# Kernel tuning notes

Hardware: AMD Instinct MI355X
Metric: run time of the kernel (lower is better)

The kernel has to match this reference:

```python
import jax, jax.numpy as jnp
import numpy as np


def setup_inputs() -> dict:
    key = jax.random.key(0)
    k1, k2 = jax.random.split(key)
    B, Lc, Lm, D = 8, 2048, 2048, 128
    context = jax.random.normal(k1, (B, Lc, D), dtype=jnp.float32)
    main = jax.random.normal(k2, (B, Lm, D), dtype=jnp.float32)
    return {"context": context, "main": main}


def reference(context, main):
    # weights[b,c,m] = sum_d context[b,c,d] * main[b,m,d]   (Keras dot axes=[2,2])
    weights = jnp.einsum("bcd,bmd->bcm", context, main)
    # K.softmax default axis=-1: normalize over the main-length axis m
    weights = jax.nn.softmax(weights, axis=-1)
    # dot([weights, context], axes=1): contract axis 1 (c) of both -> (B, Lm, D)
    weighted = jnp.einsum("bcm,bcd->bmd", weights, context)
    return main - weighted
```

## Files before the change

### kernel.cpp

```cpp
#include <hip/hip_runtime.h>


#define BATCH 8
#define L_SEQ 2048
#define DD 128
#define SHIFT 40.0f
#define LDA 136

typedef __attribute__((ext_vector_type(8))) short bf16x8;
typedef __attribute__((ext_vector_type(4))) short bf16x4;
typedef __attribute__((ext_vector_type(4))) float f32x4;
typedef __attribute__((ext_vector_type(16))) float f32x16;
typedef __attribute__((ext_vector_type(4))) unsigned int uint4v;

__device__ __forceinline__ short f2bf(float f) {
    unsigned u = __builtin_bit_cast(unsigned, f);
    return (short)((u + 0x8000u) >> 16);
}

__device__ __forceinline__ void gl2lds16(const short* g, short* l) {
    __builtin_amdgcn_global_load_lds(
        (const __attribute__((address_space(1))) unsigned int*)g,
        (__attribute__((address_space(3))) unsigned int*)l, 16, 0, 0);
}

template <int NT>
__device__ __forceinline__ void stage_tile(short* __restrict__ dst,
                                           const float* __restrict__ src,
                                           int nelts, int t) {
    for (int base = 0; base < nelts; base += NT * 8) {
        int flat = base + t * 8;
        const float4* p = (const float4*)(src + flat);
        float4 v0 = p[0];
        float4 v1 = p[1];
        bf16x8 s;
        s[0] = f2bf(v0.x); s[1] = f2bf(v0.y); s[2] = f2bf(v0.z); s[3] = f2bf(v0.w);
        s[4] = f2bf(v1.x); s[5] = f2bf(v1.y); s[6] = f2bf(v1.z); s[7] = f2bf(v1.w);
        int row = flat >> 7;
        int col = flat & 127;
        *(bf16x8*)&dst[row * LDA + col] = s;
    }
}

__global__ __launch_bounds__(256) void zero_kernel(float* __restrict__ p, int n) {
    int i = blockIdx.x * 256 + threadIdx.x;
    if (i < n) p[i] = 0.0f;
}


__global__ __launch_bounds__(256) void convert_kernel(const float* __restrict__ ctx,
                                                      const float* __restrict__ mn,
                                                      short* __restrict__ Cbf,
                                                      short* __restrict__ Mbf,
                                                      float* __restrict__ Lg) {
    int tid = blockIdx.x * 256 + threadIdx.x;
    if (tid < BATCH * L_SEQ) Lg[tid] = 0.0f;
    const int half = BATCH * L_SEQ * DD / 8;
    int id = tid;
    const float* src;
    short* dst;
    if (id < half) { src = ctx; dst = Cbf; }
    else           { id -= half; src = mn; dst = Mbf; }
    int row = id >> 4;
    int lc = id & 15;
    const float4* p = (const float4*)(src + ((size_t)row << 7) + lc * 8);
    float4 v0 = p[0];
    float4 v1 = p[1];
    bf16x8 s;
    s[0] = f2bf(v0.x); s[1] = f2bf(v0.y); s[2] = f2bf(v0.z); s[3] = f2bf(v0.w);
    s[4] = f2bf(v1.x); s[5] = f2bf(v1.y); s[6] = f2bf(v1.z); s[7] = f2bf(v1.w);
    int pc = (lc & 8) | ((lc ^ row) & 7);
    *(bf16x8*)&dst[((size_t)row << 7) + pc * 8] = s;
}

__global__ __launch_bounds__(256, 2) void stats_kernel(const short* __restrict__ Cbf,
                                                       const short* __restrict__ Mbf,
                                                       float* __restrict__ Lg) {
    __shared__ short Cs[128 * 128];
    __shared__ short Ms[2][64 * 128];

    int bid = blockIdx.x;
    int b  = bid & 7;
    int r2 = bid >> 3;
    int mc = r2 & 3;
    int ct = r2 >> 2;
    int t = threadIdx.x;
    int w = t >> 6;
    int l = t & 63;
    int a15 = l & 15;
    int q = l >> 4;
    int h = a15 & 7;
    int cw = (w & 1) * 64;
    int mw = (w >> 1) * 32;

    {
        const short* gC = Cbf + ((size_t)(b * L_SEQ + ct * 128)) * DD;
        const short* gM = Mbf + ((size_t)(b * L_SEQ + mc * 512)) * DD;
        #pragma unroll
        for (int ii = 0; ii < 8; ++ii) {
            int inst = w * 8 + ii;
            gl2lds16(gC + inst * 512 + l * 8, Cs + inst * 512);
        }
        #pragma unroll
        for (int ii = 0; ii < 4; ++ii) {
            int inst = w * 4 + ii;
            gl2lds16(gM + inst * 512 + l * 8, Ms[0] + inst * 512);
        }
    }

    __syncthreads();

    {
        const short* gM = Mbf + ((size_t)(b * L_SEQ + mc * 512 + 64)) * DD;
        #pragma unroll
        for (int ii = 0; ii < 4; ++ii) {
            int inst = w * 4 + ii;
            gl2lds16(gM + inst * 512 + l * 8, Ms[1] + inst * 512);
        }
    }

    bf16x8 af[4][4];
    #pragma unroll
    for (int ks = 0; ks < 4; ++ks) {
        int aoff = ((ks * 4 + q) ^ h) * 8;
        #pragma unroll
        for (int i = 0; i < 4; ++i)
            af[ks][i] = *(const bf16x8*)&Cs[(cw + i * 16 + a15) * 128 + aoff];
    }

    float ls[4][4] = {};

    for (int ms = 0; ms < 8; ++ms) {
        int bp = ms & 1;
        if (ms > 0) {
            __syncthreads();
            if (ms < 7) {
                const short* gM = Mbf + ((size_t)(b * L_SEQ + mc * 512 + (ms + 1) * 64)) * DD;
                #pragma unroll
                for (int ii = 0; ii < 4; ++ii) {
                    int inst = w * 4 + ii;
                    gl2lds16(gM + inst * 512 + l * 8, Ms[bp ^ 1] + inst * 512);
                }
            }
        }

        f32x4 acc[4][2];
        #pragma unroll
        for (int i = 0; i < 4; ++i)
            #pragma unroll
            for (int j = 0; j < 2; ++j) {
                f32x4 z = {0.f, 0.f, 0.f, 0.f};
                acc[i][j] = z;
            }
        #pragma unroll
        for (int ks = 0; ks < 4; ++ks) {
            int aoff = ((ks * 4 + q) ^ h) * 8;
            bf16x8 bv[2];
            #pragma unroll
            for (int j = 0; j < 2; ++j)
                bv[j] = *(const bf16x8*)&Ms[bp][(mw + j * 16 + a15) * 128 + aoff];
            #pragma unroll
            for (int i = 0; i < 4; ++i)
                #pragma unroll
                for (int j = 0; j < 2; ++j)
                    acc[i][j] = __builtin_amdgcn_mfma_f32_16x16x32_bf16(af[ks][i], bv[j], acc[i][j], 0, 0, 0);
        }

        #pragma unroll
        for (int j = 0; j < 2; ++j)
            #pragma unroll
            for (int i = 0; i < 4; ++i)
                #pragma unroll
                for (int r = 0; r < 4; ++r)
                    ls[i][r] += __expf(acc[i][j][r] - SHIFT);
    }

    #pragma unroll
    for (int i = 0; i < 4; ++i)
        #pragma unroll
        for (int r = 0; r < 4; ++r) {
            float v = ls[i][r];
            v += __shfl_xor(v, 1);
            v += __shfl_xor(v, 2);
            v += __shfl_xor(v, 4);
            v += __shfl_xor(v, 8);
            ls[i][r] = v;
        }
    if (a15 == 0) {
        #pragma unroll
        for (int i = 0; i < 4; ++i) {
            int c = ct * 128 + cw + i * 16 + q * 4;
            #pragma unroll
            for (int r = 0; r < 4; ++r)
                atomicAdd(&Lg[(size_t)b * L_SEQ + c + r], ls[i][r]);
        }
    }
}

__global__ __launch_bounds__(256) void prep_kernel(const float* __restrict__ ctx,
                                                   const float* __restrict__ Lg,
                                                   short* __restrict__ CtL) {
    __shared__ short Ts[128 * LDA];
    __shared__ float invLs[128];

    int b = blockIdx.x >> 4;
    int cc = blockIdx.x & 15;
    int t = threadIdx.x;

    if (t < 128) invLs[t] = 1.0f / Lg[(size_t)b * L_SEQ + cc * 128 + t];
    __syncthreads();

    const float* src = ctx + ((size_t)(b * L_SEQ + cc * 128)) * DD;
    #pragma unroll
    for (int i = 0; i < 8; ++i) {
        int flat = i * 2048 + t * 8;
        int r = flat >> 7;
        int c = flat & 127;
        const float4* p = (const float4*)(src + flat);
        float4 v0 = p[0];
        float4 v1 = p[1];
        float il = invLs[r];
        bf16x8 s;
        s[0] = f2bf(v0.x * il); s[1] = f2bf(v0.y * il); s[2] = f2bf(v0.z * il); s[3] = f2bf(v0.w * il);
        s[4] = f2bf(v1.x * il); s[5] = f2bf(v1.y * il); s[6] = f2bf(v1.z * il); s[7] = f2bf(v1.w * il);
        *(bf16x8*)&Ts[r * LDA + c] = s;
    }
    __syncthreads();

    int d = t >> 1;
    int ch = (t & 1) * 64;
    int key = d & 7;
    #pragma unroll
    for (int i = 0; i < 8; ++i) {
        int c = ch + i * 8;
        bf16x8 v;
        #pragma unroll
        for (int j = 0; j < 8; ++j) v[j] = Ts[(c + j) * LDA + d];
        int pc = cc * 16 + (ch >> 3) + (i ^ key);
        *(bf16x8*)&CtL[((size_t)(b * DD + d)) * L_SEQ + pc * 8] = v;
    }
}

__global__ __launch_bounds__(256, 2) void attend_fused(const short* __restrict__ Cbf,
                                                       const short* __restrict__ Mbf,
                                                       const short* __restrict__ CtL,
                                                       const float* __restrict__ mn,
                                                       float* __restrict__ out) {
    __shared__ float red[4][4096];

    int bid = blockIdx.x;
    int b = bid & 7;
    int mtile = bid >> 3;
    int t = threadIdx.x;
    int w = t >> 6;
    int l = t & 63;
    int la = l & 31;
    int hi = l >> 5;
    int ch = w;

    int m_glob = mtile * 32 + la;
    int key7 = la & 7;

    bf16x8 mf[8];
    {
        const short* mrow = Mbf + ((size_t)(b * L_SEQ + m_glob)) * DD;
        #pragma unroll
        for (int ks = 0; ks < 8; ++ks) {
            int lc = ks * 2 + hi;
            int pc = (lc & 8) | ((lc ^ key7) & 7);
            mf[ks] = *(const bf16x8*)&mrow[pc * 8];
        }
    }

    const short* gC = Cbf + ((size_t)(b * L_SEQ + ch * 32 + la)) * DD;
    const short* gT = CtL + ((size_t)(b * DD + la)) * L_SEQ;

    f32x16 o[4];
    #pragma unroll
    for (int dg = 0; dg < 4; ++dg)
        #pragma unroll
        for (int r = 0; r < 16; ++r) o[dg][r] = 0.0f;

    for (int cs = 0; cs < 16; ++cs) {
        const short* gCw = gC + (size_t)cs * 128 * DD;
        const short* gTw = gT + cs * 128;

        bf16x8 tv[4][2];
        #pragma unroll
        for (int dg = 0; dg < 4; ++dg)
            #pragma unroll
            for (int ks2 = 0; ks2 < 2; ++ks2) {
                int lc2 = ch * 4 + ks2 * 2 + hi;
                int pc2 = (lc2 & 8) | ((lc2 ^ key7) & 7);
                tv[dg][ks2] = *(const bf16x8*)&gTw[(size_t)(dg * 32) * L_SEQ + pc2 * 8];
            }

        f32x16 s;
        #pragma unroll
        for (int r = 0; r < 16; ++r) s[r] = 0.0f;
        #pragma unroll
        for (int ks = 0; ks < 8; ++ks) {
            int lc = ks * 2 + hi;
            int pc = (lc & 8) | ((lc ^ key7) & 7);
            bf16x8 av = *(const bf16x8*)&gCw[pc * 8];
            s = __builtin_amdgcn_mfma_f32_32x32x16_bf16(av, mf[ks], s, 0, 0, 0);
        }

        unsigned u[4][2];
        #pragma unroll
        for (int q = 0; q < 4; ++q)
            #pragma unroll
            for (int jj = 0; jj < 2; ++jj) {
                float e0 = __expf(s[q * 4 + jj * 2]     - SHIFT);
                float e1 = __expf(s[q * 4 + jj * 2 + 1] - SHIFT);
                u[q][jj] = ((unsigned)(unsigned short)f2bf(e1) << 16)
                         |  (unsigned)(unsigned short)f2bf(e0);
            }

        bf16x8 pa[2];
        #pragma unroll
        for (int ks2 = 0; ks2 < 2; ++ks2) {
            unsigned a0 = u[2 * ks2][0],     a1 = u[2 * ks2][1];
            unsigned b0 = u[2 * ks2 + 1][0], b1 = u[2 * ks2 + 1][1];
            unsigned a0p = (unsigned)__shfl_xor((int)a0, 32);
            unsigned a1p = (unsigned)__shfl_xor((int)a1, 32);
            unsigned b0p = (unsigned)__shfl_xor((int)b0, 32);
            unsigned b1p = (unsigned)__shfl_xor((int)b1, 32);
            uint4v pw;
            pw.x = hi ? b0p : a0;
            pw.y = hi ? b1p : a1;
            pw.z = hi ? b0  : a0p;
            pw.w = hi ? b1  : a1p;
            pa[ks2] = __builtin_bit_cast(bf16x8, pw);
        }

        #pragma unroll
        for (int dg = 0; dg < 4; ++dg)
            #pragma unroll
            for (int ks2 = 0; ks2 < 2; ++ks2)
                o[dg] = __builtin_amdgcn_mfma_f32_32x32x16_bf16(tv[dg][ks2], pa[ks2], o[dg], 0, 0, 0);
    }

    {
        float* base = red[w];
        #pragma unroll
        for (int dg = 0; dg < 4; ++dg)
            #pragma unroll
            for (int r = 0; r < 16; ++r) {
                int d = dg * 32 + (r & 3) + 8 * (r >> 2) + 4 * hi;
                base[d * 32 + la] = o[dg][r];
            }
    }
    __syncthreads();

    {
        int m  = t & 31;
        int dq = t >> 5;
        size_t gbase = ((size_t)(b * L_SEQ + mtile * 32 + m)) * DD + dq * 16;
        #pragma unroll
        for (int jq = 0; jq < 4; ++jq) {
            f32x4 v;
            #pragma unroll
            for (int e = 0; e < 4; ++e) {
                int idx = (dq * 16 + jq * 4 + e) * 32 + m;
                v[e] = red[0][idx] + red[1][idx] + red[2][idx] + red[3][idx];
            }
            f32x4 mv = *(const f32x4*)&mn[gbase + jq * 4];
            f32x4 ov;
            ov[0] = mv[0] - v[0]; ov[1] = mv[1] - v[1];
            ov[2] = mv[2] - v[2]; ov[3] = mv[3] - v[3];
            *(f32x4*)&out[gbase + jq * 4] = ov;
        }
    }
}


__global__ __launch_bounds__(256, 4) void stats_fb(const float* __restrict__ ctx,
                                                   const float* __restrict__ mn,
                                                   float* __restrict__ Lg) {
    __shared__ short Cs[64 * LDA];
    __shared__ short Ms[64 * LDA];

    int bid = blockIdx.x;
    int mc = bid & 3;
    int ct = (bid >> 2) & 31;
    int b  = bid >> 7;
    int t = threadIdx.x;
    int w = t >> 6;
    int l = t & 63;
    int a15 = l & 15;
    int q = l >> 4;

    stage_tile<256>(Cs, ctx + ((size_t)b * L_SEQ + ct * 64) * DD, 64 * DD, t);

    float ls[4] = {0.f, 0.f, 0.f, 0.f};
    for (int mt = 0; mt < 8; ++mt) {
        __syncthreads();
        int m0 = (mc * 8 + mt) * 64;
        stage_tile<256>(Ms, mn + ((size_t)b * L_SEQ + m0) * DD, 64 * DD, t);
        __syncthreads();

        f32x4 acc[4] = {{0.f,0.f,0.f,0.f},{0.f,0.f,0.f,0.f},{0.f,0.f,0.f,0.f},{0.f,0.f,0.f,0.f}};
        #pragma unroll
        for (int ks = 0; ks < 4; ++ks) {
            int k0 = ks * 32 + q * 8;
            bf16x8 a = *(const bf16x8*)&Cs[(w * 16 + a15) * LDA + k0];
            #pragma unroll
            for (int g = 0; g < 4; ++g) {
                bf16x8 bb = *(const bf16x8*)&Ms[(g * 16 + a15) * LDA + k0];
                acc[g] = __builtin_amdgcn_mfma_f32_16x16x32_bf16(a, bb, acc[g], 0, 0, 0);
            }
        }
        #pragma unroll
        for (int g = 0; g < 4; ++g)
            #pragma unroll
            for (int r = 0; r < 4; ++r)
                ls[r] += __expf(acc[g][r] - SHIFT);
    }

    #pragma unroll
    for (int r = 0; r < 4; ++r) {
        float v = ls[r];
        v += __shfl_xor(v, 1);
        v += __shfl_xor(v, 2);
        v += __shfl_xor(v, 4);
        v += __shfl_xor(v, 8);
        ls[r] = v;
    }
    if (a15 == 0) {
        int c = ct * 64 + w * 16 + q * 4;
        #pragma unroll
        for (int r = 0; r < 4; ++r)
            atomicAdd(&Lg[(size_t)b * L_SEQ + c + r], ls[r]);
    }
}

__global__ __launch_bounds__(1024, 4) void attend_fb(const float* __restrict__ ctx,
                                                     const float* __restrict__ mn,
                                                     const float* __restrict__ Lg,
                                                     float* __restrict__ out) {
    __shared__ short Mt[64 * LDA];
    __shared__ short Cs[128 * LDA];
    __shared__ short Ct[128 * LDA];
    __shared__ short Ps[64 * LDA];
    __shared__ float invLs[128];

    int bid = blockIdx.x;
    int mtile = bid & 31;
    int b = bid >> 5;
    int m0 = mtile * 64;
    int t = threadIdx.x;
    int w = t >> 6;
    int l = t & 63;
    int a15 = l & 15;
    int q = l >> 4;
    int mg = w & 3;
    int pg = w >> 2;

    stage_tile<1024>(Mt, mn + ((size_t)b * L_SEQ + m0) * DD, 64 * DD, t);

    f32x4 oacc[2] = {{0.f,0.f,0.f,0.f},{0.f,0.f,0.f,0.f}};

    for (int cs = 0; cs < 16; ++cs) {
        int c0 = cs * 128;
        __syncthreads();
        stage_tile<1024>(Cs, ctx + ((size_t)b * L_SEQ + c0) * DD, 128 * DD, t);
        if (t < 128) invLs[t] = 1.0f / Lg[(size_t)b * L_SEQ + c0 + t];
        __syncthreads();

        {
            int cc = t & 127;
            int d0 = (t >> 7) * 16;
            #pragma unroll
            for (int hh = 0; hh < 2; ++hh) {
                bf16x8 v = *(const bf16x8*)&Cs[cc * LDA + d0 + hh * 8];
                #pragma unroll
                for (int j = 0; j < 8; ++j)
                    Ct[(d0 + hh * 8 + j) * LDA + cc] = v[j];
            }
        }

        f32x4 sacc[2] = {{0.f,0.f,0.f,0.f},{0.f,0.f,0.f,0.f}};
        #pragma unroll
        for (int ks = 0; ks < 4; ++ks) {
            int k0 = ks * 32 + q * 8;
            bf16x8 a = *(const bf16x8*)&Mt[(mg * 16 + a15) * LDA + k0];
            #pragma unroll
            for (int g = 0; g < 2; ++g) {
                bf16x8 bb = *(const bf16x8*)&Cs[((pg * 2 + g) * 16 + a15) * LDA + k0];
                sacc[g] = __builtin_amdgcn_mfma_f32_16x16x32_bf16(a, bb, sacc[g], 0, 0, 0);
            }
        }
        #pragma unroll
        for (int g = 0; g < 2; ++g) {
            int cl = (pg * 2 + g) * 16 + a15;
            float il = invLs[cl];
            #pragma unroll
            for (int r = 0; r < 4; ++r) {
                float p = __expf(sacc[g][r] - SHIFT) * il;
                Ps[(mg * 16 + q * 4 + r) * LDA + cl] = f2bf(p);
            }
        }
        __syncthreads();

        #pragma unroll
        for (int ks = 0; ks < 4; ++ks) {
            int k0 = ks * 32 + q * 8;
            bf16x8 a = *(const bf16x8*)&Ps[(mg * 16 + a15) * LDA + k0];
            #pragma unroll
            for (int g = 0; g < 2; ++g) {
                bf16x8 bb = *(const bf16x8*)&Ct[((pg * 2 + g) * 16 + a15) * LDA + k0];
                oacc[g] = __builtin_amdgcn_mfma_f32_16x16x32_bf16(a, bb, oacc[g], 0, 0, 0);
            }
        }
    }

    #pragma unroll
    for (int g = 0; g < 2; ++g) {
        int dl = (pg * 2 + g) * 16 + a15;
        #pragma unroll
        for (int r = 0; r < 4; ++r) {
            int ml = mg * 16 + q * 4 + r;
            size_t idx = ((size_t)b * L_SEQ + m0 + ml) * DD + dl;
            out[idx] = mn[idx] - oacc[g][r];
        }
    }
}


extern "C" void kernel_launch(void* const* d_in, const int* in_sizes, int n_in,
                              void* d_out, int out_size, void* d_ws, size_t ws_size,
                              hipStream_t stream) {
    const float* ctx = (const float*)d_in[0];
    const float* mn  = (const float*)d_in[1];
    float* out = (float*)d_out;

    const size_t LG_BYTES = (size_t)BATCH * L_SEQ * sizeof(float);
    const size_t BF_BYTES = (size_t)BATCH * L_SEQ * DD * sizeof(short);
    const size_t NEED = LG_BYTES + 3 * BF_BYTES;

    float* Lg = (float*)d_ws;

    if (ws_size >= NEED) {
        short* Cbf = (short*)((char*)d_ws + LG_BYTES);
        short* Mbf = (short*)((char*)d_ws + LG_BYTES + BF_BYTES);
        short* CtL = (short*)((char*)d_ws + LG_BYTES + 2 * BF_BYTES);
        convert_kernel<<<2048, 256, 0, stream>>>(ctx, mn, Cbf, Mbf, Lg);
        stats_kernel<<<BATCH * 16 * 4, 256, 0, stream>>>(Cbf, Mbf, Lg);
        prep_kernel<<<BATCH * 16, 256, 0, stream>>>(ctx, Lg, CtL);
        attend_fused<<<BATCH * 64, 256, 0, stream>>>(Cbf, Mbf, CtL, mn, out);
    } else {
        int nL = BATCH * L_SEQ;
        zero_kernel<<<(nL + 255) / 256, 256, 0, stream>>>(Lg, nL);
        stats_fb<<<BATCH * 32 * 4, 256, 0, stream>>>(ctx, mn, Lg);
        attend_fb<<<BATCH * 32, 1024, 0, stream>>>(ctx, mn, Lg, out);
    }
}
```

Baseline: 124.9 us.

## Pre-pack operands into MFMA fragment layout and fold 1/L into attend

The convert kernel now writes context, main and transposed context directly in per-lane MFMA fragment order, so later kernels load fragments from global memory with contiguous vector loads instead of LDS staging and swizzled addressing. The stats kernel is rewritten around 32x32x16 MFMAs that read fragments straight from global, and it reduces per-row sums in shared memory to write 1/L without atomics or a zero pass. The separate prep kernel is removed: the 1/L scaling moves into attend_fused, where each exponent is multiplied by the loaded inverse. This removes one launch and the scaled transpose pass, at the cost of extra global fragment reads in stats (no LDS reuse of main tiles) and bf16 rounding applied after scaling rather than before.

```diff
diff --git a/kernel.cpp b/kernel.cpp
--- a/kernel.cpp
+++ b/kernel.cpp
@@ -6,9 +6,9 @@
 #define DD 128
 #define SHIFT 40.0f
 #define LDA 136
+#define TLD 136
 
 typedef __attribute__((ext_vector_type(8))) short bf16x8;
-typedef __attribute__((ext_vector_type(4))) short bf16x4;
 typedef __attribute__((ext_vector_type(4))) float f32x4;
 typedef __attribute__((ext_vector_type(16))) float f32x16;
 typedef __attribute__((ext_vector_type(4))) unsigned int uint4v;
@@ -16,12 +16,6 @@
 __device__ __forceinline__ short f2bf(float f) {
     unsigned u = __builtin_bit_cast(unsigned, f);
     return (short)((u + 0x8000u) >> 16);
-}
-
-__device__ __forceinline__ void gl2lds16(const short* g, short* l) {
-    __builtin_amdgcn_global_load_lds(
-        (const __attribute__((address_space(1))) unsigned int*)g,
-        (__attribute__((address_space(3))) unsigned int*)l, 16, 0, 0);
 }
 
 template <int NT>
@@ -50,200 +44,130 @@
 
 __global__ __launch_bounds__(256) void convert_kernel(const float* __restrict__ ctx,
                                                       const float* __restrict__ mn,
-                                                      short* __restrict__ Cbf,
-                                                      short* __restrict__ Mbf,
-                                                      float* __restrict__ Lg) {
-    int tid = blockIdx.x * 256 + threadIdx.x;
-    if (tid < BATCH * L_SEQ) Lg[tid] = 0.0f;
-    const int half = BATCH * L_SEQ * DD / 8;
-    int id = tid;
-    const float* src;
-    short* dst;
-    if (id < half) { src = ctx; dst = Cbf; }
-    else           { id -= half; src = mn; dst = Mbf; }
-    int row = id >> 4;
-    int lc = id & 15;
-    const float4* p = (const float4*)(src + ((size_t)row << 7) + lc * 8);
-    float4 v0 = p[0];
-    float4 v1 = p[1];
-    bf16x8 s;
-    s[0] = f2bf(v0.x); s[1] = f2bf(v0.y); s[2] = f2bf(v0.z); s[3] = f2bf(v0.w);
-    s[4] = f2bf(v1.x); s[5] = f2bf(v1.y); s[6] = f2bf(v1.z); s[7] = f2bf(v1.w);
-    int pc = (lc & 8) | ((lc ^ row) & 7);
-    *(bf16x8*)&dst[((size_t)row << 7) + pc * 8] = s;
-}
-
-__global__ __launch_bounds__(256, 2) void stats_kernel(const short* __restrict__ Cbf,
-                                                       const short* __restrict__ Mbf,
-                                                       float* __restrict__ Lg) {
-    __shared__ short Cs[128 * 128];
-    __shared__ short Ms[2][64 * 128];
+                                                      short* __restrict__ Cf,
+                                                      short* __restrict__ Mf,
+                                                      short* __restrict__ Ctf) {
+    __shared__ short Ts[32 * TLD];
 
     int bid = blockIdx.x;
-    int b  = bid & 7;
-    int r2 = bid >> 3;
-    int mc = r2 & 3;
-    int ct = r2 >> 2;
+    int tsel = bid & 1;
+    int b = (bid >> 1) & 7;
+    int rg = bid >> 4;
+    int t = threadIdx.x;
+
+    const float* src = (tsel ? mn : ctx) + ((size_t)(b * L_SEQ + rg * 32)) * DD;
+
+    #pragma unroll
+    for (int i = 0; i < 2; ++i) {
+        int flat = i * 2048 + t * 8;
+        int r = flat >> 7;
+        int d = flat & 127;
+        const float4* p = (const float4*)(src + flat);
+        float4 v0 = p[0];
+        float4 v1 = p[1];
+        bf16x8 s;
+        s[0] = f2bf(v0.x); s[1] = f2bf(v0.y); s[2] = f2bf(v0.z); s[3] = f2bf(v0.w);
+        s[4] = f2bf(v1.x); s[5] = f2bf(v1.y); s[6] = f2bf(v1.z); s[7] = f2bf(v1.w);
+        *(bf16x8*)&Ts[r * TLD + d] = s;
+    }
+    __syncthreads();
+
+    if (tsel == 0) {
+        int cs = rg >> 2;
+        int ch = rg & 3;
+        size_t cfb = (size_t)(((b * 16 + cs) * 4 + ch) * 8) * 512;
+        #pragma unroll
+        for (int i = 0; i < 2; ++i) {
+            int slot = i * 256 + t;
+            int ks = slot >> 6;
+            int l2 = slot & 63;
+            int la = l2 & 31;
+            int hi = l2 >> 5;
+            bf16x8 v = *(const bf16x8*)&Ts[la * TLD + (ks * 2 + hi) * 8];
+            *(bf16x8*)&Cf[cfb + (size_t)ks * 512 + l2 * 8] = v;
+        }
+        size_t ctb = (size_t)((((b * 16 + cs) * 4 + ch) * 4) * 2) * 512;
+        #pragma unroll
+        for (int i = 0; i < 2; ++i) {
+            int slot = i * 256 + t;
+            int recl = slot >> 6;
+            int l2 = slot & 63;
+            int dg = recl >> 1;
+            int ks2 = recl & 1;
+            int la = l2 & 31;
+            int hi = l2 >> 5;
+            int d = dg * 32 + la;
+            int c0 = (ks2 * 2 + hi) * 8;
+            bf16x8 v;
+            #pragma unroll
+            for (int j = 0; j < 8; ++j) v[j] = Ts[(c0 + j) * TLD + d];
+            *(bf16x8*)&Ctf[ctb + (size_t)recl * 512 + l2 * 8] = v;
+        }
+    } else {
+        size_t mfb = (size_t)((b * 64 + rg) * 8) * 512;
+        #pragma unroll
+        for (int i = 0; i < 2; ++i) {
+            int slot = i * 256 + t;
+            int ks = slot >> 6;
+            int l2 = slot & 63;
+            int la = l2 & 31;
+            int hi = l2 >> 5;
+            bf16x8 v = *(const bf16x8*)&Ts[la * TLD + (ks * 2 + hi) * 8];
+            *(bf16x8*)&Mf[mfb + (size_t)ks * 512 + l2 * 8] = v;
+        }
+    }
+}
+
+__global__ __launch_bounds__(256) void stats_kernel(const short* __restrict__ Cf,
+                                                    const short* __restrict__ Mf,
+                                                    float* __restrict__ invLg) {
+    __shared__ float red[4][32];
+
+    int bid = blockIdx.x;
+    int b = bid & 7;
+    int ct = bid >> 3;
     int t = threadIdx.x;
     int w = t >> 6;
     int l = t & 63;
-    int a15 = l & 15;
-    int q = l >> 4;
-    int h = a15 & 7;
-    int cw = (w & 1) * 64;
-    int mw = (w >> 1) * 32;
-
+    int la = l & 31;
+
+    bf16x8 cf[8];
     {
-        const short* gC = Cbf + ((size_t)(b * L_SEQ + ct * 128)) * DD;
-        const short* gM = Mbf + ((size_t)(b * L_SEQ + mc * 512)) * DD;
-        #pragma unroll
-        for (int ii = 0; ii < 8; ++ii) {
-            int inst = w * 8 + ii;
-            gl2lds16(gC + inst * 512 + l * 8, Cs + inst * 512);
-        }
-        #pragma unroll
-        for (int ii = 0; ii < 4; ++ii) {
-            int inst = w * 4 + ii;
-            gl2lds16(gM + inst * 512 + l * 8, Ms[0] + inst * 512);
-        }
-    }
-
+        const short* cfp = Cf + (size_t)(((b * 16 + (ct >> 2)) * 4 + (ct & 3)) * 8) * 512 + l * 8;
+        #pragma unroll
+        for (int ks = 0; ks < 8; ++ks)
+            cf[ks] = *(const bf16x8*)&cfp[(size_t)ks * 512];
+    }
+
+    float lacc = 0.0f;
+    for (int mw = w * 16; mw < w * 16 + 16; ++mw) {
+        const short* mfp = Mf + (size_t)((b * 64 + mw) * 8) * 512 + l * 8;
+        f32x16 s;
+        #pragma unroll
+        for (int r = 0; r < 16; ++r) s[r] = 0.0f;
+        #pragma unroll
+        for (int ks = 0; ks < 8; ++ks) {
+            bf16x8 av = *(const bf16x8*)&mfp[(size_t)ks * 512];
+            s = __builtin_amdgcn_mfma_f32_32x32x16_bf16(av, cf[ks], s, 0, 0, 0);
+        }
+        #pragma unroll
+        for (int r = 0; r < 16; ++r)
+            lacc += __expf(s[r] - SHIFT);
+    }
+
+    lacc += __shfl_xor(lacc, 32);
+    if (l < 32) red[w][la] = lacc;
     __syncthreads();
-
-    {
-        const short* gM = Mbf + ((size_t)(b * L_SEQ + mc * 512 + 64)) * DD;
-        #pragma unroll
-        for (int ii = 0; ii < 4; ++ii) {
-            int inst = w * 4 + ii;
-            gl2lds16(gM + inst * 512 + l * 8, Ms[1] + inst * 512);
-        }
-    }
-
-    bf16x8 af[4][4];
-    #pragma unroll
-    for (int ks = 0; ks < 4; ++ks) {
-        int aoff = ((ks * 4 + q) ^ h) * 8;
-        #pragma unroll
-        for (int i = 0; i < 4; ++i)
-            af[ks][i] = *(const bf16x8*)&Cs[(cw + i * 16 + a15) * 128 + aoff];
-    }
-
-    float ls[4][4] = {};
-
-    for (int ms = 0; ms < 8; ++ms) {
-        int bp = ms & 1;
-        if (ms > 0) {
-            __syncthreads();
-            if (ms < 7) {
-                const short* gM = Mbf + ((size_t)(b * L_SEQ + mc * 512 + (ms + 1) * 64)) * DD;
-                #pragma unroll
-                for (int ii = 0; ii < 4; ++ii) {
-                    int inst = w * 4 + ii;
-                    gl2lds16(gM + inst * 512 + l * 8, Ms[bp ^ 1] + inst * 512);
-                }
-            }
-        }
-
-        f32x4 acc[4][2];
-        #pragma unroll
-        for (int i = 0; i < 4; ++i)
-            #pragma unroll
-            for (int j = 0; j < 2; ++j) {
-                f32x4 z = {0.f, 0.f, 0.f, 0.f};
-                acc[i][j] = z;
-            }
-        #pragma unroll
-        for (int ks = 0; ks < 4; ++ks) {
-            int aoff = ((ks * 4 + q) ^ h) * 8;
-            bf16x8 bv[2];
-            #pragma unroll
-            for (int j = 0; j < 2; ++j)
-                bv[j] = *(const bf16x8*)&Ms[bp][(mw + j * 16 + a15) * 128 + aoff];
-            #pragma unroll
-            for (int i = 0; i < 4; ++i)
-                #pragma unroll
-                for (int j = 0; j < 2; ++j)
-                    acc[i][j] = __builtin_amdgcn_mfma_f32_16x16x32_bf16(af[ks][i], bv[j], acc[i][j], 0, 0, 0);
-        }
-
-        #pragma unroll
-        for (int j = 0; j < 2; ++j)
-            #pragma unroll
-            for (int i = 0; i < 4; ++i)
-                #pragma unroll
-                for (int r = 0; r < 4; ++r)
-                    ls[i][r] += __expf(acc[i][j][r] - SHIFT);
-    }
-
-    #pragma unroll
-    for (int i = 0; i < 4; ++i)
-        #pragma unroll
-        for (int r = 0; r < 4; ++r) {
-            float v = ls[i][r];
-            v += __shfl_xor(v, 1);
-            v += __shfl_xor(v, 2);
-            v += __shfl_xor(v, 4);
-            v += __shfl_xor(v, 8);
-            ls[i][r] = v;
-        }
-    if (a15 == 0) {
-        #pragma unroll
-        for (int i = 0; i < 4; ++i) {
-            int c = ct * 128 + cw + i * 16 + q * 4;
-            #pragma unroll
-            for (int r = 0; r < 4; ++r)
-                atomicAdd(&Lg[(size_t)b * L_SEQ + c + r], ls[i][r]);
-        }
-    }
-}
-
-__global__ __launch_bounds__(256) void prep_kernel(const float* __restrict__ ctx,
-                                                   const float* __restrict__ Lg,
-                                                   short* __restrict__ CtL) {
-    __shared__ short Ts[128 * LDA];
-    __shared__ float invLs[128];
-
-    int b = blockIdx.x >> 4;
-    int cc = blockIdx.x & 15;
-    int t = threadIdx.x;
-
-    if (t < 128) invLs[t] = 1.0f / Lg[(size_t)b * L_SEQ + cc * 128 + t];
-    __syncthreads();
-
-    const float* src = ctx + ((size_t)(b * L_SEQ + cc * 128)) * DD;
-    #pragma unroll
-    for (int i = 0; i < 8; ++i) {
-        int flat = i * 2048 + t * 8;
-        int r = flat >> 7;
-        int c = flat & 127;
-        const float4* p = (const float4*)(src + flat);
-        float4 v0 = p[0];
-        float4 v1 = p[1];
-        float il = invLs[r];
-        bf16x8 s;
-        s[0] = f2bf(v0.x * il); s[1] = f2bf(v0.y * il); s[2] = f2bf(v0.z * il); s[3] = f2bf(v0.w * il);
-        s[4] = f2bf(v1.x * il); s[5] = f2bf(v1.y * il); s[6] = f2bf(v1.z * il); s[7] = f2bf(v1.w * il);
-        *(bf16x8*)&Ts[r * LDA + c] = s;
-    }
-    __syncthreads();
-
-    int d = t >> 1;
-    int ch = (t & 1) * 64;
-    int key = d & 7;
-    #pragma unroll
-    for (int i = 0; i < 8; ++i) {
-        int c = ch + i * 8;
-        bf16x8 v;
-        #pragma unroll
-        for (int j = 0; j < 8; ++j) v[j] = Ts[(c + j) * LDA + d];
-        int pc = cc * 16 + (ch >> 3) + (i ^ key);
-        *(bf16x8*)&CtL[((size_t)(b * DD + d)) * L_SEQ + pc * 8] = v;
-    }
-}
-
-__global__ __launch_bounds__(256, 2) void attend_fused(const short* __restrict__ Cbf,
-                                                       const short* __restrict__ Mbf,
-                                                       const short* __restrict__ CtL,
+    if (t < 32) {
+        float L = red[0][t] + red[1][t] + red[2][t] + red[3][t];
+        invLg[(size_t)b * L_SEQ + ct * 32 + t] = 1.0f / L;
+    }
+}
+
+__global__ __launch_bounds__(256, 2) void attend_fused(const short* __restrict__ Cf,
+                                                       const short* __restrict__ Mf,
+                                                       const short* __restrict__ Ctf,
+                                                       const float* __restrict__ invLg,
                                                        const float* __restrict__ mn,
                                                        float* __restrict__ out) {
     __shared__ float red[4][4096];
@@ -258,22 +182,13 @@
     int hi = l >> 5;
     int ch = w;
 
-    int m_glob = mtile * 32 + la;
-    int key7 = la & 7;
-
     bf16x8 mf[8];
     {
-        const short* mrow = Mbf + ((size_t)(b * L_SEQ + m_glob)) * DD;
-        #pragma unroll
-        for (int ks = 0; ks < 8; ++ks) {
-            int lc = ks * 2 + hi;
-            int pc = (lc & 8) | ((lc ^ key7) & 7);
-            mf[ks] = *(const bf16x8*)&mrow[pc * 8];
-        }
-    }
-
-    const short* gC = Cbf + ((size_t)(b * L_SEQ + ch * 32 + la)) * DD;
-    const short* gT = CtL + ((size_t)(b * DD + la)) * L_SEQ;
+        const short* mfp = Mf + (size_t)((b * 64 + mtile) * 8) * 512 + l * 8;
+        #pragma unroll
+        for (int ks = 0; ks < 8; ++ks)
+            mf[ks] = *(const bf16x8*)&mfp[(size_t)ks * 512];
+    }
 
     f32x16 o[4];
     #pragma unroll
@@ -281,28 +196,30 @@
         #pragma unroll
         for (int r = 0; r < 16; ++r) o[dg][r] = 0.0f;
 
+    const float* ilbase = invLg + (size_t)b * L_SEQ + ch * 32 + hi * 4;
+
     for (int cs = 0; cs < 16; ++cs) {
-        const short* gCw = gC + (size_t)cs * 128 * DD;
-        const short* gTw = gT + cs * 128;
+        const short* cfp = Cf + (size_t)(((b * 16 + cs) * 4 + ch) * 8) * 512 + l * 8;
+        const short* tfp = Ctf + (size_t)((((b * 16 + cs) * 4 + ch) * 4) * 2) * 512 + l * 8;
 
         bf16x8 tv[4][2];
         #pragma unroll
         for (int dg = 0; dg < 4; ++dg)
             #pragma unroll
-            for (int ks2 = 0; ks2 < 2; ++ks2) {
-                int lc2 = ch * 4 + ks2 * 2 + hi;
-                int pc2 = (lc2 & 8) | ((lc2 ^ key7) & 7);
-                tv[dg][ks2] = *(const bf16x8*)&gTw[(size_t)(dg * 32) * L_SEQ + pc2 * 8];
-            }
+            for (int ks2 = 0; ks2 < 2; ++ks2)
+                tv[dg][ks2] = *(const bf16x8*)&tfp[(size_t)(dg * 2 + ks2) * 512];
+
+        f32x4 ilv[4];
+        #pragma unroll
+        for (int q = 0; q < 4; ++q)
+            ilv[q] = *(const f32x4*)&ilbase[cs * 128 + q * 8];
 
         f32x16 s;
         #pragma unroll
         for (int r = 0; r < 16; ++r) s[r] = 0.0f;
         #pragma unroll
         for (int ks = 0; ks < 8; ++ks) {
-            int lc = ks * 2 + hi;
-            int pc = (lc & 8) | ((lc ^ key7) & 7);
-            bf16x8 av = *(const bf16x8*)&gCw[pc * 8];
+            bf16x8 av = *(const bf16x8*)&cfp[(size_t)ks * 512];
             s = __builtin_amdgcn_mfma_f32_32x32x16_bf16(av, mf[ks], s, 0, 0, 0);
         }
 
@@ -311,8 +228,8 @@
         for (int q = 0; q < 4; ++q)
             #pragma unroll
             for (int jj = 0; jj < 2; ++jj) {
-                float e0 = __expf(s[q * 4 + jj * 2]     - SHIFT);
-                float e1 = __expf(s[q * 4 + jj * 2 + 1] - SHIFT);
+                float e0 = __expf(s[q * 4 + jj * 2]     - SHIFT) * ilv[q][jj * 2];
+                float e1 = __expf(s[q * 4 + jj * 2 + 1] - SHIFT) * ilv[q][jj * 2 + 1];
                 u[q][jj] = ((unsigned)(unsigned short)f2bf(e1) << 16)
                          |  (unsigned)(unsigned short)f2bf(e0);
             }
@@ -542,13 +459,12 @@
     float* Lg = (float*)d_ws;
 
     if (ws_size >= NEED) {
-        short* Cbf = (short*)((char*)d_ws + LG_BYTES);
-        short* Mbf = (short*)((char*)d_ws + LG_BYTES + BF_BYTES);
-        short* CtL = (short*)((char*)d_ws + LG_BYTES + 2 * BF_BYTES);
-        convert_kernel<<<2048, 256, 0, stream>>>(ctx, mn, Cbf, Mbf, Lg);
-        stats_kernel<<<BATCH * 16 * 4, 256, 0, stream>>>(Cbf, Mbf, Lg);
-        prep_kernel<<<BATCH * 16, 256, 0, stream>>>(ctx, Lg, CtL);
-        attend_fused<<<BATCH * 64, 256, 0, stream>>>(Cbf, Mbf, CtL, mn, out);
+        short* Cf  = (short*)((char*)d_ws + LG_BYTES);
+        short* Mf  = (short*)((char*)d_ws + LG_BYTES + BF_BYTES);
+        short* Ctf = (short*)((char*)d_ws + LG_BYTES + 2 * BF_BYTES);
+        convert_kernel<<<1024, 256, 0, stream>>>(ctx, mn, Cf, Mf, Ctf);
+        stats_kernel<<<512, 256, 0, stream>>>(Cf, Mf, Lg);
+        attend_fused<<<512, 256, 0, stream>>>(Cf, Mf, Ctf, Lg, mn, out);
     } else {
         int nL = BATCH * L_SEQ;
         zero_kernel<<<(nL + 255) / 256, 256, 0, stream>>>(Lg, nL);
```

New measurement: 121.4 us. -2.8%, faster.
